# Performance work log

Measured on AMD Instinct MI355X. Metric: run time of the kernel, lower is better.

Reference implementation:

```python
import jax, jax.numpy as jnp
import numpy as np
import math

B, L, D, H = 2, 2048, 1024, 16
DH = D // H  # 64


def setup_inputs() -> dict:
    key = jax.random.key(0)
    ks = jax.random.split(key, 8)
    s = 1.0 / math.sqrt(D)
    return {
        "query": jax.random.normal(ks[0], (B, L, D), dtype=jnp.float32),
        "key": jax.random.normal(ks[1], (B, L, D), dtype=jnp.float32),
        "value": jax.random.normal(ks[2], (B, L, D), dtype=jnp.float32),
        "attn_mask": jax.random.bernoulli(ks[3], 0.1, (B, L, L)),  # True = masked
        "Wq": jax.random.normal(ks[4], (D, D), dtype=jnp.float32) * s,
        "Wk": jax.random.normal(ks[5], (D, D), dtype=jnp.float32) * s,
        "Wv": jax.random.normal(ks[6], (D, D), dtype=jnp.float32) * s,
        "Wo": jax.random.normal(ks[7], (D, D), dtype=jnp.float32) * s,
    }


def reference(query, key, value, attn_mask, Wq, Wk, Wv, Wo):
    # torch nn.Linear computes x @ W.T (bias=False here)
    def shape(x):
        b, l, _ = x.shape
        return x.reshape(b, l, H, DH).transpose(0, 2, 1, 3)  # [B,H,L,DH]

    q = shape(query @ Wq.T) / jnp.sqrt(jnp.float32(DH))
    k = shape(key @ Wk.T)
    v = shape(value @ Wv.T)

    scores = jnp.einsum("bhqd,bhkd->bhqk", q, k)  # [B,H,Q,K]
    if attn_mask is not None:
        scores = jnp.where(attn_mask[:, None, :, :], jnp.float32(-1e18), scores)
    attn = jax.nn.softmax(scores, axis=-1)
    # dropout p=0.0 (eval/deterministic) -> identity
    context = jnp.einsum("bhqk,bhkd->bhqd", attn, v)
    context = context.transpose(0, 2, 1, 3).reshape(query.shape[0], -1, D)
    output = context @ Wo.T
    top_attn = attn[:, 0, :, :]
    return output, top_attn
```

## Files before the change

kernel.cpp:

```cpp
#include <hip/hip_runtime.h>

#define BB 2
#define LL 2048
#define DD 1024
#define HH 16
#define DHH 64

typedef _Float16 f16;
typedef _Float16 f16x8 __attribute__((ext_vector_type(8)));
typedef _Float16 f16x4 __attribute__((ext_vector_type(4)));
typedef _Float16 f16x2 __attribute__((ext_vector_type(2)));
typedef float f32x4 __attribute__((ext_vector_type(4)));
typedef unsigned long long u64;

#define VWAIT(N) asm volatile("s_waitcnt vmcnt(" #N ")" ::: "memory")
#define SB0() __builtin_amdgcn_sched_barrier(0)

__device__ __forceinline__ void gload_lds16(const void* g, void* l) {
    __builtin_amdgcn_global_load_lds(
        (const __attribute__((address_space(1))) void*)g,
        (__attribute__((address_space(3))) void*)l, 16, 0, 0);
}

__device__ __forceinline__ f16x4 cvt4f(float4 v) {
    f16x4 o;
    o[0] = (f16)v.x; o[1] = (f16)v.y; o[2] = (f16)v.z; o[3] = (f16)v.w;
    return o;
}

__global__ void prep(const float* __restrict__ q, const float* __restrict__ k,
                     const float* __restrict__ v, const int* __restrict__ msk,
                     const float* __restrict__ wq, const float* __restrict__ wk,
                     const float* __restrict__ wv, const float* __restrict__ wo,
                     f16* __restrict__ bufQ, f16* __restrict__ bufK, f16* __restrict__ bufV,
                     f16* __restrict__ wh, u64* __restrict__ Mp, float scq) {
    const int tid = threadIdx.x;
    const int y = blockIdx.y;
    if (y == 0) {
        const int lane = tid & 63;
        int w = (blockIdx.x * 256 + tid) >> 6;
        const int nw = (1024 * 256) >> 6;
        for (; w < BB * LL * 32; w += nw) {
            int mv = msk[(size_t)w * 64 + lane];
            u64 bits = __ballot(mv != 0);
            if (lane == 0) {
                const int kt = w & 31;
                const int bq = w >> 5;
                const int qq = bq & 2047, b = bq >> 11;
                Mp[((size_t)b * 32 + kt) * LL + qq] = bits;
            }
        }
    } else if (y == 1) {
        int i = blockIdx.x * 256 + tid;
        const int stride = 1024 * 256;
        for (; i < 4 * 262144; i += stride) {
            const int sel = i >> 18, j = i & 262143;
            const float* s = sel == 0 ? wq : sel == 1 ? wk : sel == 2 ? wv : wo;
            ((f16x4*)wh)[i] = cvt4f(((const float4*)s)[j]);
        }
    } else {
        const float* s = y == 2 ? q : y == 3 ? k : v;
        f16* o = y == 2 ? bufQ : y == 3 ? bufK : bufV;
        const float sc = y == 2 ? scq : 1.0f;
        int i = blockIdx.x * 256 + tid;
        const int stride = 1024 * 256;
        for (; i < (int)(BB * LL * DD / 4); i += stride) {
            float4 vv = ((const float4*)s)[i];
            vv.x *= sc; vv.y *= sc; vv.z *= sc; vv.w *= sc;
            ((f16x4*)o)[i] = cvt4f(vv);
        }
    }
}

__global__ void cvt_kernel(const float* __restrict__ src, f16* __restrict__ dst, int n4, float sc) {
    int i = blockIdx.x * blockDim.x + threadIdx.x;
    const int stride = gridDim.x * blockDim.x;
    for (; i < n4; i += stride) {
        float4 v = ((const float4*)src)[i];
        v.x *= sc; v.y *= sc; v.z *= sc; v.w *= sc;
        ((f16x4*)dst)[i] = cvt4f(v);
    }
}
__global__ void cvt4_kernel(const float* __restrict__ a, const float* __restrict__ b,
                            const float* __restrict__ c, const float* __restrict__ d,
                            f16* __restrict__ dst, int n4) {
    const float* s = blockIdx.y == 0 ? a : blockIdx.y == 1 ? b : blockIdx.y == 2 ? c : d;
    f16* o = dst + (size_t)blockIdx.y * n4 * 4;
    int i = blockIdx.x * blockDim.x + threadIdx.x;
    const int stride = gridDim.x * blockDim.x;
    for (; i < n4; i += stride)
        ((f16x4*)o)[i] = cvt4f(((const float4*)s)[i]);
}
__global__ void pack_mask(const int* __restrict__ mask, u64* __restrict__ out, int nwords) {
    const int lane = threadIdx.x & 63;
    int w = (blockIdx.x * blockDim.x + threadIdx.x) >> 6;
    const int nw = (gridDim.x * blockDim.x) >> 6;
    for (; w < nwords; w += nw) {
        int mv = mask[(size_t)w * 64 + lane];
        u64 bits = __ballot(mv != 0);
        if (lane == 0) {
            const int kt = w & 31;
            const int bq = w >> 5;
            const int qq = bq & 2047, b = bq >> 11;
            out[((size_t)b * 32 + kt) * LL + qq] = bits;
        }
    }
}

__device__ __forceinline__ void gemm_core(const f16* __restrict__ A, const f16* __restrict__ W,
                                          f16* __restrict__ C, int z, int xb, int yb, char* lds) {
    const int tid = threadIdx.x, wid = tid >> 6, lane = tid & 63;
    const int m0 = yb * 128, n0 = xb * 128;
    const int lq = lane & 15, lg = lane >> 4;
    const int wm = (wid >> 1) << 6, wn = (wid & 1) << 6;
    f32x4 acc[4][4] = {};

    for (int kt = 0; kt < 32; ++kt) {
        #pragma unroll
        for (int j = 0; j < 2; ++j) {
            const int ldsoff = (wid * 2 + j) << 10;
            const int o = ldsoff + lane * 16;
            const int row = o >> 6;
            const int c8 = (o >> 4) & 3;
            gload_lds16(A + (size_t)(m0 + row) * DD + kt * 32 + c8 * 8, lds + ldsoff);
            gload_lds16(W + (size_t)(n0 + row) * DD + kt * 32 + c8 * 8, lds + 8192 + ldsoff);
        }
        __syncthreads();
        f16x8 af[4], bf[4];
        #pragma unroll
        for (int m = 0; m < 4; ++m)
            af[m] = *(const f16x8*)(lds + (wm + m * 16 + lq) * 64 + lg * 16);
        #pragma unroll
        for (int n = 0; n < 4; ++n)
            bf[n] = *(const f16x8*)(lds + 8192 + (wn + n * 16 + lq) * 64 + lg * 16);
        #pragma unroll
        for (int m = 0; m < 4; ++m)
            #pragma unroll
            for (int n = 0; n < 4; ++n)
                acc[m][n] = __builtin_amdgcn_mfma_f32_16x16x32_f16(af[m], bf[n], acc[m][n], 0, 0, 0);
        __syncthreads();
    }

    #pragma unroll
    for (int m = 0; m < 4; ++m)
        #pragma unroll
        for (int n = 0; n < 4; ++n)
            #pragma unroll
            for (int r = 0; r < 4; ++r) {
                const int row = m0 + wm + m * 16 + lg * 4 + r;
                const int col = n0 + wn + n * 16 + lq;
                const float val = acc[m][n][r];
                if (z < 2) {
                    C[(size_t)row * DD + col] = (f16)val;
                } else {
                    const int b = row >> 11, l = row & 2047;
                    const int h = col >> 6, dh = col & 63;
                    C[((size_t)((b * HH + h) * DHH + dh) << 11) + l] = (f16)val;
                }
            }
}

__global__ __launch_bounds__(256) void gemm_qkv(
        const f16* __restrict__ A0, const f16* __restrict__ A1, const f16* __restrict__ A2,
        const f16* __restrict__ W0, const f16* __restrict__ W1, const f16* __restrict__ W2,
        f16* __restrict__ C0, f16* __restrict__ C1, f16* __restrict__ C2) {
    __shared__ __align__(16) char lds[16384];
    const int bid = blockIdx.x;
    const int xcd = bid & 7, j = bid >> 3;
    const int p = xcd * 12 + (j >> 3);
    const int xb = j & 7;
    const int z = p >> 5, yb = p & 31;
    const f16* A = z == 0 ? A0 : z == 1 ? A1 : A2;
    const f16* W = z == 0 ? W0 : z == 1 ? W1 : W2;
    f16* C       = z == 0 ? C0 : z == 1 ? C1 : C2;
    gemm_core(A, W, C, z, xb, yb, lds);
}

__global__ __launch_bounds__(256) void gemm_one(const f16* __restrict__ A, const f16* __restrict__ W,
                                                f16* __restrict__ C, int z) {
    __shared__ __align__(16) char lds[16384];
    gemm_core(A, W, C, z, blockIdx.x, blockIdx.y, lds);
}

__global__ __launch_bounds__(256) void gemm_out(const f16* __restrict__ A, const f16* __restrict__ W,
                                                float* __restrict__ C) {
    __shared__ __align__(16) char lds[12288];
    const int bid = blockIdx.x;
    const int xcd = bid & 7, j = bid >> 3;
    const int yb = xcd * 4 + (j >> 4);
    const int xb = j & 15;
    const int tid = threadIdx.x, wid = tid >> 6, lane = tid & 63;
    const int m0 = yb * 128, n0 = xb * 64;
    const int lq = lane & 15, lg = lane >> 4;
    const int wm = wid * 32;
    f32x4 acc[2][4] = {};

    for (int kt = 0; kt < 32; ++kt) {
        #pragma unroll
        for (int j2 = 0; j2 < 2; ++j2) {
            const int o = (j2 * 256 + tid) * 16;
            const int row = o >> 6, c8 = (o >> 4) & 3;
            gload_lds16(A + (size_t)(m0 + row) * DD + kt * 32 + c8 * 8,
                        lds + j2 * 4096 + (wid << 10));
        }
        {
            const int o = tid * 16;
            const int row = o >> 6, c8 = (o >> 4) & 3;
            gload_lds16(W + (size_t)(n0 + row) * DD + kt * 32 + c8 * 8,
                        lds + 8192 + (wid << 10));
        }
        __syncthreads();
        f16x8 af[2], bf[4];
        #pragma unroll
        for (int m = 0; m < 2; ++m)
            af[m] = *(const f16x8*)(lds + (wm + m * 16 + lq) * 64 + lg * 16);
        #pragma unroll
        for (int n = 0; n < 4; ++n)
            bf[n] = *(const f16x8*)(lds + 8192 + (n * 16 + lq) * 64 + lg * 16);
        #pragma unroll
        for (int m = 0; m < 2; ++m)
            #pragma unroll
            for (int n = 0; n < 4; ++n)
                acc[m][n] = __builtin_amdgcn_mfma_f32_16x16x32_f16(af[m], bf[n], acc[m][n], 0, 0, 0);
        __syncthreads();
    }

    #pragma unroll
    for (int m = 0; m < 2; ++m)
        #pragma unroll
        for (int n = 0; n < 4; ++n)
            #pragma unroll
            for (int r = 0; r < 4; ++r) {
                const int row = m0 + wm + m * 16 + lg * 4 + r;
                const int col = n0 + n * 16 + lq;
                C[(size_t)row * DD + col] = acc[m][n][r];
            }
}

template<bool TOPF16>
__global__ __launch_bounds__(256) void attn_fwd(const f16* __restrict__ Qp, const f16* __restrict__ Kp,
                                                const f16* __restrict__ VTp,
                                                const u64* __restrict__ Mp,
                                                f16* __restrict__ Op, void* __restrict__ topout,
                                                float* __restrict__ statsLinv) {
    extern __shared__ char lds[];
    const int tid = threadIdx.x, wid = tid >> 6, lane = tid & 63;
    const int lq = lane & 15, lg = lane >> 4;
    const int bid = blockIdx.x;
    const int xcd = bid & 7, j = bid >> 3;
    const int bh = xcd * 4 + (j >> 5);
    const int qt = j & 31;
    const int b = bh >> 4, h = bh & 15;
    const bool topblk = (h == 0);
    const int qrow = qt * 64 + wid * 16 + lq;

    f16x8 qf[2];
    #pragma unroll
    for (int kk = 0; kk < 2; ++kk)
        qf[kk] = *(const f16x8*)(Qp + (size_t)(b * LL + qrow) * DD + h * 64 + (kk * 4 + lg) * 8);

    {
        #pragma unroll
        for (int jj = 0; jj < 2; ++jj) {
            const int o = (wid * 2 + jj) * 1024 + lane * 16;
            const int row = o >> 7, sc = ((o >> 4) & 7) ^ (row & 7);
            gload_lds16(Kp + (size_t)(b * LL + row) * DD + h * 64 + sc * 8,
                        lds + 8192 + (wid * 2 + jj) * 1024);
            gload_lds16(VTp + (size_t)((b * HH + h) * DHH + row) * LL + sc * 8,
                        lds + 24576 + (wid * 2 + jj) * 1024);
        }
    }

    float lsum = 0.f;
    f32x4 acc[4] = {};

    for (int kt = 0; kt < 32; ++kt) {
        if (topblk && kt > 0) { VWAIT(4); } else { VWAIT(0); }
        SB0();
        __builtin_amdgcn_s_barrier();
        SB0();
        const u64 cm = Mp[((size_t)b * 32 + kt) * LL + qrow];
        SB0();
        {
            const int nk = (kt + 1 < 32) ? kt + 1 : 31;
            const int nb = (kt + 1) & 1;
            #pragma unroll
            for (int jj = 0; jj < 2; ++jj) {
                const int o = (wid * 2 + jj) * 1024 + lane * 16;
                const int row = o >> 7, sc = ((o >> 4) & 7) ^ (row & 7);
                gload_lds16(Kp + (size_t)(b * LL + nk * 64 + row) * DD + h * 64 + sc * 8,
                            lds + 8192 + nb * 8192 + (wid * 2 + jj) * 1024);
                gload_lds16(VTp + (size_t)((b * HH + h) * DHH + row) * LL + nk * 64 + sc * 8,
                            lds + 24576 + nb * 8192 + (wid * 2 + jj) * 1024);
            }
        }
        SB0();

        const int cb = kt & 1;
        const char* Kb = lds + 8192 + cb * 8192;
        const char* Vb = lds + 24576 + cb * 8192;

        f32x4 s[4] = {};
        __builtin_amdgcn_s_setprio(1);
        #pragma unroll
        for (int f = 0; f < 4; ++f)
            #pragma unroll
            for (int kk = 0; kk < 2; ++kk) {
                const int co = (((kk * 4 + lg) ^ (lq & 7)) << 4);
                f16x8 kf = *(const f16x8*)(Kb + (f * 16 + lq) * 128 + co);
                s[f] = __builtin_amdgcn_mfma_f32_16x16x32_f16(kf, qf[kk], s[f], 0, 0, 0);
            }
        __builtin_amdgcn_s_setprio(0);

        const u64 wsh = cm >> (lg * 4);
        const unsigned lo = (unsigned)wsh, hi = (unsigned)(wsh >> 32);
        f16x4 ph[4];
        #pragma unroll
        for (int f = 0; f < 4; ++f) {
            const unsigned nib = ((f < 2) ? (lo >> (f * 16)) : (hi >> ((f - 2) * 16))) & 0xFu;
            #pragma unroll
            for (int r = 0; r < 4; ++r)
                if (nib & (1u << r)) s[f][r] = -1e18f;
            const float p0 = __builtin_amdgcn_exp2f(s[f][0]);
            const float p1 = __builtin_amdgcn_exp2f(s[f][1]);
            const float p2 = __builtin_amdgcn_exp2f(s[f][2]);
            const float p3 = __builtin_amdgcn_exp2f(s[f][3]);
            lsum += (p0 + p1) + (p2 + p3);
            f16x2 pa = __builtin_bit_cast(f16x2, __builtin_amdgcn_cvt_pkrtz(p0, p1));
            f16x2 pb = __builtin_bit_cast(f16x2, __builtin_amdgcn_cvt_pkrtz(p2, p3));
            ph[f][0] = pa[0]; ph[f][1] = pa[1]; ph[f][2] = pb[0]; ph[f][3] = pb[1];
        }

        if (topblk) {
            if (TOPF16) {
                f16* T = (f16*)topout;
                #pragma unroll
                for (int f = 0; f < 4; ++f)
                    *(f16x4*)(T + ((size_t)b * LL + qrow) * LL + kt * 64 + f * 16 + lg * 4) = ph[f];
            } else {
                float* T = (float*)topout;
                #pragma unroll
                for (int f = 0; f < 4; ++f)
                    *(f32x4*)(T + ((size_t)b * LL + qrow) * LL + kt * 64 + f * 16 + lg * 4) = s[f];
            }
        }

        #pragma unroll
        for (int f = 0; f < 4; ++f) {
            const int chunk = f * 2 + (lg >> 1);
            const int bo = ((chunk ^ (lq & 7)) << 4) + (lg & 1) * 8;
            *(f16x4*)(lds + (wid << 11) + lq * 128 + bo) = ph[f];
        }

        __builtin_amdgcn_s_setprio(1);
        #pragma unroll
        for (int kk = 0; kk < 2; ++kk) {
            const int co = (((kk * 4 + lg) ^ (lq & 7)) << 4);
            f16x8 pf = *(const f16x8*)(lds + (wid << 11) + lq * 128 + co);
            #pragma unroll
            for (int f = 0; f < 4; ++f) {
                f16x8 vf = *(const f16x8*)(Vb + (f * 16 + lq) * 128 + co);
                acc[f] = __builtin_amdgcn_mfma_f32_16x16x32_f16(vf, pf, acc[f], 0, 0, 0);
            }
        }
        __builtin_amdgcn_s_setprio(0);
    }

    lsum += __shfl_xor(lsum, 16);
    lsum += __shfl_xor(lsum, 32);
    const float linv = 1.f / lsum;
    #pragma unroll
    for (int f = 0; f < 4; ++f) {
        f16x4 ov;
        #pragma unroll
        for (int r = 0; r < 4; ++r) ov[r] = (f16)(acc[f][r] * linv);
        *(f16x4*)(Op + (size_t)(b * LL + qrow) * DD + h * 64 + f * 16 + lg * 4) = ov;
    }
    if (topblk && lg == 0) statsLinv[(size_t)b * LL + qrow] = linv;
}

template<bool TOPF16>
__global__ void norm_top(float* __restrict__ top, const void* __restrict__ src,
                         const float* __restrict__ linvp, int n) {
    int i = blockIdx.x * blockDim.x + threadIdx.x;
    const int stride = gridDim.x * blockDim.x;
    if (TOPF16) {
        const f16x8* s8 = (const f16x8*)src;
        for (; i < n; i += stride) {
            f16x8 v = s8[i];
            const float linv = linvp[(i * 8) >> 11];
            float4 a, bq;
            a.x = (float)v[0] * linv; a.y = (float)v[1] * linv;
            a.z = (float)v[2] * linv; a.w = (float)v[3] * linv;
            bq.x = (float)v[4] * linv; bq.y = (float)v[5] * linv;
            bq.z = (float)v[6] * linv; bq.w = (float)v[7] * linv;
            ((float4*)top)[i * 2] = a;
            ((float4*)top)[i * 2 + 1] = bq;
        }
    } else {
        for (; i < n; i += stride) {
            float4 v = ((const float4*)top)[i];
            const float linv = linvp[(i * 4) >> 11];
            v.x = __builtin_amdgcn_exp2f(v.x) * linv;
            v.y = __builtin_amdgcn_exp2f(v.y) * linv;
            v.z = __builtin_amdgcn_exp2f(v.z) * linv;
            v.w = __builtin_amdgcn_exp2f(v.w) * linv;
            ((float4*)top)[i] = v;
        }
    }
}

extern "C" void kernel_launch(void* const* d_in, const int* in_sizes, int n_in,
                              void* d_out, int out_size, void* d_ws, size_t ws_size,
                              hipStream_t stream) {
    const float* q   = (const float*)d_in[0];
    const float* k   = (const float*)d_in[1];
    const float* v   = (const float*)d_in[2];
    const int*   msk = (const int*)d_in[3];
    const float* wq  = (const float*)d_in[4];
    const float* wk  = (const float*)d_in[5];
    const float* wv  = (const float*)d_in[6];
    const float* wo  = (const float*)d_in[7];
    float* out = (float*)d_out;

    const size_t NX = (size_t)BB * LL * DD;
    const size_t NW = (size_t)DD * DD;
    const int NMW = BB * LL * (LL / 64);
    const size_t NXo = NX;
    const float SCQ = 0.125f * 1.4426950408889634f;
    const int ALDS = 40960;

    f16* ws = (f16*)d_ws;
    const size_t needed = (6 * NX + 4 * NW) * 2 + (size_t)NMW * 8 + (size_t)BB * LL * 4;
    const bool fused = ws_size >= needed;

    if (fused) {
        f16* bufQ = ws;
        f16* bufK = bufQ + NX;
        f16* bufV = bufK + NX;
        f16* topP = bufK;
        f16* wh   = bufV + NX;
        f16* wqh = wh, *wkh = wh + NW, *wvh = wh + 2 * NW, *woh = wh + 3 * NW;
        f16* Qp  = wh + 4 * NW;
        f16* Kp  = Qp + NX;
        f16* VTp = Kp + NX;
        u64* Mp  = (u64*)(VTp + NX);
        float* statsLinv = (float*)(Mp + NMW);

        prep<<<dim3(1024, 5), 256, 0, stream>>>(q, k, v, msk, wq, wk, wv, wo,
                                                bufQ, bufK, bufV, wh, Mp, SCQ);
        gemm_qkv<<<768, 256, 0, stream>>>(bufQ, bufK, bufV, wqh, wkh, wvh, Qp, Kp, VTp);
        attn_fwd<true><<<1024, 256, ALDS, stream>>>(Qp, Kp, VTp, Mp, bufQ, topP, statsLinv);
        norm_top<true><<<2048, 256, 0, stream>>>(out + NXo, topP, statsLinv,
                                                 (int)((size_t)BB * LL * LL / 8));
        gemm_out<<<512, 256, 0, stream>>>(bufQ, woh, out);
    } else {
        f16* bufA = ws;
        f16* wh   = bufA + NX;
        f16* wqh = wh, *wkh = wh + NW, *wvh = wh + 2 * NW, *woh = wh + 3 * NW;
        f16* Qp  = wh + 4 * NW;
        f16* Kp  = Qp + NX;
        f16* VTp = Kp + NX;
        u64* Mp  = (u64*)(VTp + NX);
        float* statsLinv = (float*)(Mp + NMW);

        pack_mask<<<256, 256, 0, stream>>>(msk, Mp, NMW);
        cvt4_kernel<<<dim3(128, 4), 256, 0, stream>>>(wq, wk, wv, wo, wh, (int)(NW / 4));
        cvt_kernel<<<2048, 256, 0, stream>>>(q, bufA, (int)(NX / 4), SCQ);
        gemm_one<<<dim3(8, 32), 256, 0, stream>>>(bufA, wqh, Qp, 0);
        cvt_kernel<<<2048, 256, 0, stream>>>(k, bufA, (int)(NX / 4), 1.f);
        gemm_one<<<dim3(8, 32), 256, 0, stream>>>(bufA, wkh, Kp, 1);
        cvt_kernel<<<2048, 256, 0, stream>>>(v, bufA, (int)(NX / 4), 1.f);
        gemm_one<<<dim3(8, 32), 256, 0, stream>>>(bufA, wvh, VTp, 2);
        attn_fwd<false><<<1024, 256, ALDS, stream>>>(Qp, Kp, VTp, Mp, bufA,
                                                     out + NXo, statsLinv);
        norm_top<false><<<2048, 256, 0, stream>>>(out + NXo, out + NXo, statsLinv,
                                                  (int)((size_t)BB * LL * LL / 4));
        gemm_out<<<512, 256, 0, stream>>>(bufA, woh, out);
    }
}
```

Measured before the change: 167.7 us.

## Triple-buffer LDS with prefetch depth two in projection GEMMs

Replaces the load-sync-compute-sync loop in the QKV and output projection GEMMs with a three-stage LDS ring buffer. Tiles are prefetched two iterations ahead using direct global-to-LDS loads, and each iteration waits with a partial vmcnt and a single barrier. MFMA sections are wrapped in s_setprio to favour compute waves. The aim is to hide global memory latency behind MFMA work, at the cost of roughly triple the LDS per block, which may lower occupancy. It also issues redundant tail loads of the last tile to keep the vmcnt accounting uniform.

```diff
diff --git a/kernel.cpp b/kernel.cpp
--- a/kernel.cpp
+++ b/kernel.cpp
@@ -115,30 +115,55 @@
     const int wm = (wid >> 1) << 6, wn = (wid & 1) << 6;
     f32x4 acc[4][4] = {};
 
-    for (int kt = 0; kt < 32; ++kt) {
+    #pragma unroll
+    for (int t = 0; t < 2; ++t)
         #pragma unroll
         for (int j = 0; j < 2; ++j) {
             const int ldsoff = (wid * 2 + j) << 10;
             const int o = ldsoff + lane * 16;
-            const int row = o >> 6;
-            const int c8 = (o >> 4) & 3;
-            gload_lds16(A + (size_t)(m0 + row) * DD + kt * 32 + c8 * 8, lds + ldsoff);
-            gload_lds16(W + (size_t)(n0 + row) * DD + kt * 32 + c8 * 8, lds + 8192 + ldsoff);
-        }
-        __syncthreads();
+            const int row = o >> 6, c8 = (o >> 4) & 3;
+            gload_lds16(A + (size_t)(m0 + row) * DD + t * 32 + c8 * 8, lds + t * 8192 + ldsoff);
+            gload_lds16(W + (size_t)(n0 + row) * DD + t * 32 + c8 * 8, lds + 24576 + t * 8192 + ldsoff);
+        }
+
+    for (int kt = 0; kt < 32; ++kt) {
+        VWAIT(4);
+        SB0();
+        __builtin_amdgcn_s_barrier();
+        SB0();
+        {
+            const int nk = (kt + 2 < 32) ? kt + 2 : 31;
+            const int nb = (kt + 2) % 3;
+            #pragma unroll
+            for (int j = 0; j < 2; ++j) {
+                const int ldsoff = (wid * 2 + j) << 10;
+                const int o = ldsoff + lane * 16;
+                const int row = o >> 6, c8 = (o >> 4) & 3;
+                gload_lds16(A + (size_t)(m0 + row) * DD + nk * 32 + c8 * 8,
+                            lds + nb * 8192 + ldsoff);
+                gload_lds16(W + (size_t)(n0 + row) * DD + nk * 32 + c8 * 8,
+                            lds + 24576 + nb * 8192 + ldsoff);
+            }
+        }
+        SB0();
+
+        const int cb = kt % 3;
+        const char* Ab = lds + cb * 8192;
+        const char* Bb = lds + 24576 + cb * 8192;
         f16x8 af[4], bf[4];
         #pragma unroll
         for (int m = 0; m < 4; ++m)
-            af[m] = *(const f16x8*)(lds + (wm + m * 16 + lq) * 64 + lg * 16);
+            af[m] = *(const f16x8*)(Ab + (wm + m * 16 + lq) * 64 + lg * 16);
         #pragma unroll
         for (int n = 0; n < 4; ++n)
-            bf[n] = *(const f16x8*)(lds + 8192 + (wn + n * 16 + lq) * 64 + lg * 16);
+            bf[n] = *(const f16x8*)(Bb + (wn + n * 16 + lq) * 64 + lg * 16);
+        __builtin_amdgcn_s_setprio(1);
         #pragma unroll
         for (int m = 0; m < 4; ++m)
             #pragma unroll
             for (int n = 0; n < 4; ++n)
                 acc[m][n] = __builtin_amdgcn_mfma_f32_16x16x32_f16(af[m], bf[n], acc[m][n], 0, 0, 0);
-        __syncthreads();
+        __builtin_amdgcn_s_setprio(0);
     }
 
     #pragma unroll
@@ -164,7 +189,7 @@
         const f16* __restrict__ A0, const f16* __restrict__ A1, const f16* __restrict__ A2,
         const f16* __restrict__ W0, const f16* __restrict__ W1, const f16* __restrict__ W2,
         f16* __restrict__ C0, f16* __restrict__ C1, f16* __restrict__ C2) {
-    __shared__ __align__(16) char lds[16384];
+    __shared__ __align__(16) char lds[49152];
     const int bid = blockIdx.x;
     const int xcd = bid & 7, j = bid >> 3;
     const int p = xcd * 12 + (j >> 3);
@@ -178,13 +203,13 @@
 
 __global__ __launch_bounds__(256) void gemm_one(const f16* __restrict__ A, const f16* __restrict__ W,
                                                 f16* __restrict__ C, int z) {
-    __shared__ __align__(16) char lds[16384];
+    __shared__ __align__(16) char lds[49152];
     gemm_core(A, W, C, z, blockIdx.x, blockIdx.y, lds);
 }
 
 __global__ __launch_bounds__(256) void gemm_out(const f16* __restrict__ A, const f16* __restrict__ W,
                                                 float* __restrict__ C) {
-    __shared__ __align__(16) char lds[12288];
+    __shared__ __align__(16) char lds[36864];
     const int bid = blockIdx.x;
     const int xcd = bid & 7, j = bid >> 3;
     const int yb = xcd * 4 + (j >> 4);
@@ -195,34 +220,64 @@
     const int wm = wid * 32;
     f32x4 acc[2][4] = {};
 
-    for (int kt = 0; kt < 32; ++kt) {
+    #pragma unroll
+    for (int t = 0; t < 2; ++t) {
         #pragma unroll
         for (int j2 = 0; j2 < 2; ++j2) {
             const int o = (j2 * 256 + tid) * 16;
             const int row = o >> 6, c8 = (o >> 4) & 3;
-            gload_lds16(A + (size_t)(m0 + row) * DD + kt * 32 + c8 * 8,
-                        lds + j2 * 4096 + (wid << 10));
+            gload_lds16(A + (size_t)(m0 + row) * DD + t * 32 + c8 * 8,
+                        lds + t * 8192 + j2 * 4096 + (wid << 10));
         }
         {
             const int o = tid * 16;
             const int row = o >> 6, c8 = (o >> 4) & 3;
-            gload_lds16(W + (size_t)(n0 + row) * DD + kt * 32 + c8 * 8,
-                        lds + 8192 + (wid << 10));
-        }
-        __syncthreads();
+            gload_lds16(W + (size_t)(n0 + row) * DD + t * 32 + c8 * 8,
+                        lds + 24576 + t * 4096 + (wid << 10));
+        }
+    }
+
+    for (int kt = 0; kt < 32; ++kt) {
+        VWAIT(3);
+        SB0();
+        __builtin_amdgcn_s_barrier();
+        SB0();
+        {
+            const int nk = (kt + 2 < 32) ? kt + 2 : 31;
+            const int nb = (kt + 2) % 3;
+            #pragma unroll
+            for (int j2 = 0; j2 < 2; ++j2) {
+                const int o = (j2 * 256 + tid) * 16;
+                const int row = o >> 6, c8 = (o >> 4) & 3;
+                gload_lds16(A + (size_t)(m0 + row) * DD + nk * 32 + c8 * 8,
+                            lds + nb * 8192 + j2 * 4096 + (wid << 10));
+            }
+            {
+                const int o = tid * 16;
+                const int row = o >> 6, c8 = (o >> 4) & 3;
+                gload_lds16(W + (size_t)(n0 + row) * DD + nk * 32 + c8 * 8,
+                            lds + 24576 + nb * 4096 + (wid << 10));
+            }
+        }
+        SB0();
+
+        const int cb = kt % 3;
+        const char* Ab = lds + cb * 8192;
+        const char* Bb = lds + 24576 + cb * 4096;
         f16x8 af[2], bf[4];
         #pragma unroll
         for (int m = 0; m < 2; ++m)
-            af[m] = *(const f16x8*)(lds + (wm + m * 16 + lq) * 64 + lg * 16);
+            af[m] = *(const f16x8*)(Ab + (wm + m * 16 + lq) * 64 + lg * 16);
         #pragma unroll
         for (int n = 0; n < 4; ++n)
-            bf[n] = *(const f16x8*)(lds + 8192 + (n * 16 + lq) * 64 + lg * 16);
+            bf[n] = *(const f16x8*)(Bb + (n * 16 + lq) * 64 + lg * 16);
+        __builtin_amdgcn_s_setprio(1);
         #pragma unroll
         for (int m = 0; m < 2; ++m)
             #pragma unroll
             for (int n = 0; n < 4; ++n)
                 acc[m][n] = __builtin_amdgcn_mfma_f32_16x16x32_f16(af[m], bf[n], acc[m][n], 0, 0, 0);
-        __syncthreads();
+        __builtin_amdgcn_s_setprio(0);
     }
 
     #pragma unroll
```

Measured after the change: 167.0 us. About the same (-0.4%).
